# Kernel optimization log

Measured on AMD Instinct MI355X. Metric: run time of the kernel, lower is better.

## Reference

```python
import jax, jax.numpy as jnp
import numpy as np

INPUT_SIZE = 64
HIDDEN_SIZE = 512
OUTPUT_SIZE = 1
BATCH = 128
SEQ = 1024


def setup_inputs() -> dict:
    key = jax.random.key(0)
    ks = jax.random.split(key, 7)
    H, I, O = HIDDEN_SIZE, INPUT_SIZE, OUTPUT_SIZE
    s = 1.0 / np.sqrt(H)  # PyTorch LSTM init scale
    x = jax.random.normal(ks[0], (BATCH, SEQ, I), dtype=jnp.float32)
    W_ih = jax.random.uniform(ks[1], (4 * H, I), minval=-s, maxval=s, dtype=jnp.float32)
    W_hh = jax.random.uniform(ks[2], (4 * H, H), minval=-s, maxval=s, dtype=jnp.float32)
    b_ih = jax.random.uniform(ks[3], (4 * H,), minval=-s, maxval=s, dtype=jnp.float32)
    b_hh = jax.random.uniform(ks[4], (4 * H,), minval=-s, maxval=s, dtype=jnp.float32)
    W_fc = jax.random.uniform(ks[5], (O, H), minval=-s, maxval=s, dtype=jnp.float32)
    b_fc = jax.random.uniform(ks[6], (O,), minval=-s, maxval=s, dtype=jnp.float32)
    return {"x": x, "W_ih": W_ih, "W_hh": W_hh, "b_ih": b_ih, "b_hh": b_hh,
            "W_fc": W_fc, "b_fc": b_fc}


def _lstm(x, W_ih, W_hh, b_ih, b_hh):
    # x: [B, T, I]; gate order in PyTorch is (i, f, g, o) along the 4H axis.
    B = x.shape[0]
    H = W_hh.shape[1]
    # Precompute input contribution for all timesteps: [B, T, 4H] -> [T, B, 4H]
    xW = jnp.einsum('bti,gi->btg', x, W_ih) + b_ih + b_hh
    xW = jnp.swapaxes(xW, 0, 1)

    def step(carry, xt):
        h, c = carry
        gates = xt + h @ W_hh.T  # [B, 4H]
        i, f, g, o = jnp.split(gates, 4, axis=-1)
        i = jax.nn.sigmoid(i)
        f = jax.nn.sigmoid(f)
        g = jnp.tanh(g)
        o = jax.nn.sigmoid(o)
        c = f * c + i * g
        h = o * jnp.tanh(c)
        return (h, c), h

    h0 = jnp.zeros((B, H), dtype=x.dtype)
    c0 = jnp.zeros((B, H), dtype=x.dtype)
    _, h_seq = jax.lax.scan(step, (h0, c0), xW)  # [T, B, H]
    return jnp.swapaxes(h_seq, 0, 1)  # [B, T, H]


def reference(x, W_ih, W_hh, b_ih, b_hh, W_fc, b_fc):
    h = _lstm(x, W_ih, W_hh, b_ih, b_hh)          # [B, T, H]
    return jnp.einsum('bth,oh->bto', h, W_fc) + b_fc  # [B, T, O]
```

## Files before the change

### kernel.cpp

```cpp
#include <hip/hip_runtime.h>

#define BB 128
#define TT 1024
#define II 64
#define HH 512
#define KK 576
#define NBLK 256
#define NTHR 256

__global__ __launch_bounds__(NTHR, 1)
void lstm_persist(const float* __restrict__ x,
                  const float* __restrict__ W_ih,
                  const float* __restrict__ W_hh,
                  const float* __restrict__ b_ih,
                  const float* __restrict__ b_hh,
                  const float* __restrict__ W_fc,
                  const float* __restrict__ b_fc,
                  float* __restrict__ out,
                  float* __restrict__ hbuf,
                  unsigned* __restrict__ bar)
{
    __shared__ float Wl[8][KK];
    __shared__ float vx[BB][68];
    __shared__ float gl[8][BB];
    __shared__ float yl[2][BB];
    __shared__ float wfc[HH];
    __shared__ float bias[8];

    const int u  = threadIdx.x;
    const int g  = blockIdx.x;
    const int j0 = g << 1;

    unsigned epoch = 0;
    unsigned* __restrict__ subc   = bar + ((g & 7) << 5);
    unsigned* __restrict__ master = bar + 256;

    for (int r = 0; r < 8; ++r) {
        const int R = (r >> 1) * HH + j0 + (r & 1);
        for (int k = u; k < KK; k += NTHR)
            Wl[r][k] = (k < II) ? W_ih[(size_t)R * II + k]
                                : W_hh[(size_t)R * HH + (k - II)];
    }
    if (u < 8) {
        const int R = (u >> 1) * HH + j0 + (u & 1);
        bias[u] = b_ih[R] + b_hh[R];
    }
    for (int k = u; k < HH; k += NTHR) wfc[k] = W_fc[k];
    if (u < BB) {
        hbuf[(size_t)u * HH + j0]     = 0.f;
        hbuf[(size_t)u * HH + j0 + 1] = 0.f;
    }

    const float bfc = b_fc[0];
    const bool  doy = (g == 0);
    const int   bA  = u & 63, bB2 = bA + 64;
    const int   rp  = u >> 6;
    const int   rA  = rp << 1, rB = rA + 1;
    const int   ub  = u & 127, ujj = u >> 7;
    float creg = 0.f;
    float4 rx[8];

#define BAR_ARRIVE() do { __threadfence(); __syncthreads();                        \
    if (u == 0) {                                                                  \
        unsigned old = __hip_atomic_fetch_add(subc, 1u, __ATOMIC_ACQ_REL,          \
                                              __HIP_MEMORY_SCOPE_AGENT);           \
        if ((old & 31u) == 31u)                                                    \
            __hip_atomic_fetch_add(master, 1u, __ATOMIC_RELEASE,                   \
                                   __HIP_MEMORY_SCOPE_AGENT);                      \
    } ++epoch; } while (0)

#define BAR_WAIT() do {                                                            \
    if (u == 0) {                                                                  \
        while (__hip_atomic_load(master, __ATOMIC_RELAXED,                         \
                                 __HIP_MEMORY_SCOPE_AGENT) < (epoch << 3))         \
            __builtin_amdgcn_s_sleep(1);                                           \
    } __syncthreads(); __threadfence(); } while (0)

    BAR_ARRIVE();
    #pragma unroll
    for (int r8 = 0; r8 < 8; ++r8) {
        const int flat = u + NTHR * r8, b = flat >> 4, q = flat & 15;
        rx[r8] = *(const float4*)(x + ((size_t)b * TT + 0) * II + (q << 2));
    }
    BAR_WAIT();

    for (int t = 0; t < TT; ++t) {
        const float* __restrict__ hsrc = hbuf + (size_t)(t & 1) * BB * HH;
        float*       __restrict__ hdst = hbuf + (size_t)((t + 1) & 1) * BB * HH;

        float a00 = 0.f, a01 = 0.f, a10 = 0.f, a11 = 0.f;
        float yacc = 0.f;

        for (int ch = 0; ch < 9; ++ch) {
            __syncthreads();
            #pragma unroll
            for (int r8 = 0; r8 < 8; ++r8) {
                const int flat = u + NTHR * r8, b = flat >> 4, q = flat & 15;
                *(float4*)&vx[b][q << 2] = rx[r8];
            }
            if (ch < 8) {
                const int k0 = ch << 6;
                #pragma unroll
                for (int r8 = 0; r8 < 8; ++r8) {
                    const int flat = u + NTHR * r8, b = flat >> 4, q = flat & 15;
                    rx[r8] = *(const float4*)(hsrc + (size_t)b * HH + k0 + (q << 2));
                }
            }
            __syncthreads();

            {
                const float* __restrict__ wra = &Wl[rA][ch << 6];
                const float* __restrict__ wrb = &Wl[rB][ch << 6];
                const float* __restrict__ va  = &vx[bA][0];
                const float* __restrict__ vb  = &vx[bB2][0];
                #pragma unroll
                for (int k4 = 0; k4 < 16; ++k4) {
                    const float4 wa = *(const float4*)(wra + (k4 << 2));
                    const float4 wb = *(const float4*)(wrb + (k4 << 2));
                    const float4 pa = *(const float4*)(va + (k4 << 2));
                    const float4 pb = *(const float4*)(vb + (k4 << 2));
                    a00 += wa.x*pa.x + wa.y*pa.y + wa.z*pa.z + wa.w*pa.w;
                    a01 += wa.x*pb.x + wa.y*pb.y + wa.z*pb.z + wa.w*pb.w;
                    a10 += wb.x*pa.x + wb.y*pa.y + wb.z*pa.z + wb.w*pa.w;
                    a11 += wb.x*pb.x + wb.y*pb.y + wb.z*pb.z + wb.w*pb.w;
                }
            }
            if (doy && t > 0 && ch > 0) {
                const float* __restrict__ wf = &wfc[((ch - 1) << 6) + (ujj << 5)];
                const float* __restrict__ vv = &vx[ub][ujj << 5];
                #pragma unroll
                for (int k4 = 0; k4 < 8; ++k4) {
                    const float4 f4 = *(const float4*)(wf + (k4 << 2));
                    const float4 v4 = *(const float4*)(vv + (k4 << 2));
                    yacc += f4.x*v4.x + f4.y*v4.y + f4.z*v4.z + f4.w*v4.w;
                }
            }
        }

        if (doy && t > 0) yl[ujj][ub] = yacc;
        gl[rA][bA]  = a00 + bias[rA];
        gl[rA][bB2] = a01 + bias[rA];
        gl[rB][bA]  = a10 + bias[rB];
        gl[rB][bB2] = a11 + bias[rB];
        __syncthreads();

        {
            const float gi = gl[0 + ujj][ub];
            const float gf = gl[2 + ujj][ub];
            const float gg = gl[4 + ujj][ub];
            const float go = gl[6 + ujj][ub];
            const float si = 1.f / (1.f + expf(-gi));
            const float sf = 1.f / (1.f + expf(-gf));
            const float tg = tanhf(gg);
            const float so = 1.f / (1.f + expf(-go));
            const float c  = sf * creg + si * tg;
            creg = c;
            hdst[(size_t)ub * HH + j0 + ujj] = so * tanhf(c);
            if (doy && t > 0 && u < BB)
                out[(size_t)u * TT + (t - 1)] = yl[0][u] + yl[1][u] + bfc;
        }

        BAR_ARRIVE();
        if (t + 1 < TT) {
            #pragma unroll
            for (int r8 = 0; r8 < 8; ++r8) {
                const int flat = u + NTHR * r8, b = flat >> 4, q = flat & 15;
                rx[r8] = *(const float4*)(x + ((size_t)b * TT + (t + 1)) * II + (q << 2));
            }
        }
        BAR_WAIT();
    }

    if (doy) {
        const float* __restrict__ hsrc = hbuf + (size_t)(TT & 1) * BB * HH;
        float yacc = 0.f;
        for (int ch = 1; ch < 9; ++ch) {
            const int k0 = (ch - 1) << 6;
            __syncthreads();
            #pragma unroll
            for (int r8 = 0; r8 < 8; ++r8) {
                const int flat = u + NTHR * r8, b = flat >> 4, q = flat & 15;
                *(float4*)&vx[b][q << 2] =
                    *(const float4*)(hsrc + (size_t)b * HH + k0 + (q << 2));
            }
            __syncthreads();
            const float* __restrict__ wf = &wfc[((ch - 1) << 6) + (ujj << 5)];
            const float* __restrict__ vv = &vx[ub][ujj << 5];
            #pragma unroll
            for (int k4 = 0; k4 < 8; ++k4) {
                const float4 f4 = *(const float4*)(wf + (k4 << 2));
                const float4 v4 = *(const float4*)(vv + (k4 << 2));
                yacc += f4.x*v4.x + f4.y*v4.y + f4.z*v4.z + f4.w*v4.w;
            }
        }
        yl[ujj][ub] = yacc;
        __syncthreads();
        if (u < BB) out[(size_t)u * TT + (TT - 1)] = yl[0][u] + yl[1][u] + bfc;
    }
#undef BAR_ARRIVE
#undef BAR_WAIT
}

extern "C" void kernel_launch(void* const* d_in, const int* in_sizes, int n_in,
                              void* d_out, int out_size, void* d_ws, size_t ws_size,
                              hipStream_t stream) {
    (void)in_sizes; (void)n_in; (void)out_size; (void)ws_size;
    const float* x    = (const float*)d_in[0];
    const float* W_ih = (const float*)d_in[1];
    const float* W_hh = (const float*)d_in[2];
    const float* b_ih = (const float*)d_in[3];
    const float* b_hh = (const float*)d_in[4];
    const float* W_fc = (const float*)d_in[5];
    const float* b_fc = (const float*)d_in[6];
    float* out = (float*)d_out;

    unsigned* bar  = (unsigned*)d_ws;
    float*    hbuf = (float*)((char*)d_ws + 4096);

    hipMemsetAsync(d_ws, 0, 4096, stream);

    void* args[] = {(void*)&x, (void*)&W_ih, (void*)&W_hh, (void*)&b_ih,
                    (void*)&b_hh, (void*)&W_fc, (void*)&b_fc, (void*)&out,
                    (void*)&hbuf, (void*)&bar};
    hipError_t e = hipLaunchCooperativeKernel((const void*)lstm_persist,
                                              dim3(NBLK), dim3(NTHR), args, 0, stream);
    if (e != hipSuccess) {
        hipLaunchKernelGGL(lstm_persist, dim3(NBLK), dim3(NTHR), 0, stream,
                           x, W_ih, W_hh, b_ih, b_hh, W_fc, b_fc, out, hbuf, bar);
    }
}
```

Baseline: 82.62 ms.

## Replace hierarchical atomic grid barrier with per-block flags and transpose h buffer

Swaps the two-level atomic counter barrier for per-block epoch flags: each block publishes its step count, and every thread polls one block's flag, which drops the serialized arrive/master chain. The hidden state buffer becomes [H][B] with relaxed agent-scope atomic loads and stores, so each thread reads 32 coalesced values per chunk into ping-pong registers. The h zero-init moves to a host memset. Relaxed atomics with no explicit fences may leave memory ordering between blocks under-specified, and the extra per-element atomic loads could cost bandwidth.

Result: slower. 315.3 ms (+281.7%).

```diff
diff --git a/kernel.cpp b/kernel.cpp
--- a/kernel.cpp
+++ b/kernel.cpp
@@ -7,6 +7,8 @@
 #define KK 576
 #define NBLK 256
 #define NTHR 256
+
+typedef unsigned int u32;
 
 __global__ __launch_bounds__(NTHR, 1)
 void lstm_persist(const float* __restrict__ x,
@@ -18,7 +20,7 @@
                   const float* __restrict__ b_fc,
                   float* __restrict__ out,
                   float* __restrict__ hbuf,
-                  unsigned* __restrict__ bar)
+                  u32*   __restrict__ flags)
 {
     __shared__ float Wl[8][KK];
     __shared__ float vx[BB][68];
@@ -31,10 +33,6 @@
     const int g  = blockIdx.x;
     const int j0 = g << 1;
 
-    unsigned epoch = 0;
-    unsigned* __restrict__ subc   = bar + ((g & 7) << 5);
-    unsigned* __restrict__ master = bar + 256;
-
     for (int r = 0; r < 8; ++r) {
         const int R = (r >> 1) * HH + j0 + (r & 1);
         for (int k = u; k < KK; k += NTHR)
@@ -46,10 +44,6 @@
         bias[u] = b_ih[R] + b_hh[R];
     }
     for (int k = u; k < HH; k += NTHR) wfc[k] = W_fc[k];
-    if (u < BB) {
-        hbuf[(size_t)u * HH + j0]     = 0.f;
-        hbuf[(size_t)u * HH + j0 + 1] = 0.f;
-    }
 
     const float bfc = b_fc[0];
     const bool  doy = (g == 0);
@@ -57,85 +51,75 @@
     const int   rp  = u >> 6;
     const int   rA  = rp << 1, rB = rA + 1;
     const int   ub  = u & 127, ujj = u >> 7;
+    const int   xb  = u >> 4, xq = u & 15;
+    const int   b2  = u & 127;
+    const int   kk0 = (u >> 7) << 5;
     float creg = 0.f;
-    float4 rx[8];
-
-#define BAR_ARRIVE() do { __threadfence(); __syncthreads();                        \
-    if (u == 0) {                                                                  \
-        unsigned old = __hip_atomic_fetch_add(subc, 1u, __ATOMIC_ACQ_REL,          \
-                                              __HIP_MEMORY_SCOPE_AGENT);           \
-        if ((old & 31u) == 31u)                                                    \
-            __hip_atomic_fetch_add(master, 1u, __ATOMIC_RELEASE,                   \
-                                   __HIP_MEMORY_SCOPE_AGENT);                      \
-    } ++epoch; } while (0)
-
-#define BAR_WAIT() do {                                                            \
-    if (u == 0) {                                                                  \
-        while (__hip_atomic_load(master, __ATOMIC_RELAXED,                         \
-                                 __HIP_MEMORY_SCOPE_AGENT) < (epoch << 3))         \
-            __builtin_amdgcn_s_sleep(1);                                           \
-    } __syncthreads(); __threadfence(); } while (0)
-
-    BAR_ARRIVE();
-    #pragma unroll
-    for (int r8 = 0; r8 < 8; ++r8) {
-        const int flat = u + NTHR * r8, b = flat >> 4, q = flat & 15;
-        rx[r8] = *(const float4*)(x + ((size_t)b * TT + 0) * II + (q << 2));
-    }
-    BAR_WAIT();
+    float4 rx4[8];
+    float  rhA[32], rhB[32];
+
+#define LOAD_X(T) { _Pragma("unroll")                                             \
+    for (int r8 = 0; r8 < 8; ++r8)                                                \
+        rx4[r8] = *(const float4*)(x + ((size_t)(xb + 16*r8) * TT + (T)) * II     \
+                                     + (xq << 2)); }
+
+#define STAGE_X { _Pragma("unroll")                                               \
+    for (int r8 = 0; r8 < 8; ++r8)                                                \
+        *(float4*)&vx[xb + 16*r8][xq << 2] = rx4[r8]; }
+
+#define LOAD_H(R, N) { const float* hp_ = hsrc + ((size_t)(((N)-1) << 6) + kk0) * BB + b2; \
+    _Pragma("unroll")                                                             \
+    for (int i = 0; i < 32; ++i)                                                  \
+        (R)[i] = __hip_atomic_load(hp_ + (size_t)i * BB, __ATOMIC_RELAXED,        \
+                                   __HIP_MEMORY_SCOPE_AGENT); }
+
+#define STAGE_H(R) { _Pragma("unroll")                                            \
+    for (int j = 0; j < 8; ++j) {                                                 \
+        float4 f_; f_.x=(R)[4*j]; f_.y=(R)[4*j+1]; f_.z=(R)[4*j+2]; f_.w=(R)[4*j+3]; \
+        *(float4*)&vx[b2][kk0 + (j << 2)] = f_; } }
+
+#define COMPUTE(CH) {                                                             \
+    const float* wra_ = &Wl[rA][(CH) << 6];                                       \
+    const float* wrb_ = &Wl[rB][(CH) << 6];                                       \
+    const float* va_  = &vx[bA][0];                                               \
+    const float* vb_  = &vx[bB2][0];                                              \
+    _Pragma("unroll")                                                             \
+    for (int k4 = 0; k4 < 16; ++k4) {                                             \
+        const float4 wa = *(const float4*)(wra_ + (k4 << 2));                     \
+        const float4 wb = *(const float4*)(wrb_ + (k4 << 2));                     \
+        const float4 pa = *(const float4*)(va_ + (k4 << 2));                      \
+        const float4 pb = *(const float4*)(vb_ + (k4 << 2));                      \
+        a00 += wa.x*pa.x + wa.y*pa.y + wa.z*pa.z + wa.w*pa.w;                     \
+        a01 += wa.x*pb.x + wa.y*pb.y + wa.z*pb.z + wa.w*pb.w;                     \
+        a10 += wb.x*pa.x + wb.y*pa.y + wb.z*pa.z + wb.w*pa.w;                     \
+        a11 += wb.x*pb.x + wb.y*pb.y + wb.z*pb.z + wb.w*pb.w; } }
+
+#define YPART(CH) if (doy && t > 0) {                                             \
+    const float* wf_ = &wfc[(((CH)-1) << 6) + (ujj << 5)];                        \
+    const float* vv_ = &vx[ub][ujj << 5];                                         \
+    _Pragma("unroll")                                                             \
+    for (int k4 = 0; k4 < 8; ++k4) {                                              \
+        const float4 f4 = *(const float4*)(wf_ + (k4 << 2));                      \
+        const float4 v4 = *(const float4*)(vv_ + (k4 << 2));                      \
+        yacc += f4.x*v4.x + f4.y*v4.y + f4.z*v4.z + f4.w*v4.w; } }
+
+    LOAD_X(0);
 
     for (int t = 0; t < TT; ++t) {
-        const float* __restrict__ hsrc = hbuf + (size_t)(t & 1) * BB * HH;
-        float*       __restrict__ hdst = hbuf + (size_t)((t + 1) & 1) * BB * HH;
-
-        float a00 = 0.f, a01 = 0.f, a10 = 0.f, a11 = 0.f;
-        float yacc = 0.f;
-
-        for (int ch = 0; ch < 9; ++ch) {
-            __syncthreads();
-            #pragma unroll
-            for (int r8 = 0; r8 < 8; ++r8) {
-                const int flat = u + NTHR * r8, b = flat >> 4, q = flat & 15;
-                *(float4*)&vx[b][q << 2] = rx[r8];
-            }
-            if (ch < 8) {
-                const int k0 = ch << 6;
-                #pragma unroll
-                for (int r8 = 0; r8 < 8; ++r8) {
-                    const int flat = u + NTHR * r8, b = flat >> 4, q = flat & 15;
-                    rx[r8] = *(const float4*)(hsrc + (size_t)b * HH + k0 + (q << 2));
-                }
-            }
-            __syncthreads();
-
-            {
-                const float* __restrict__ wra = &Wl[rA][ch << 6];
-                const float* __restrict__ wrb = &Wl[rB][ch << 6];
-                const float* __restrict__ va  = &vx[bA][0];
-                const float* __restrict__ vb  = &vx[bB2][0];
-                #pragma unroll
-                for (int k4 = 0; k4 < 16; ++k4) {
-                    const float4 wa = *(const float4*)(wra + (k4 << 2));
-                    const float4 wb = *(const float4*)(wrb + (k4 << 2));
-                    const float4 pa = *(const float4*)(va + (k4 << 2));
-                    const float4 pb = *(const float4*)(vb + (k4 << 2));
-                    a00 += wa.x*pa.x + wa.y*pa.y + wa.z*pa.z + wa.w*pa.w;
-                    a01 += wa.x*pb.x + wa.y*pb.y + wa.z*pb.z + wa.w*pb.w;
-                    a10 += wb.x*pa.x + wb.y*pa.y + wb.z*pa.z + wb.w*pa.w;
-                    a11 += wb.x*pb.x + wb.y*pb.y + wb.z*pb.z + wb.w*pb.w;
-                }
-            }
-            if (doy && t > 0 && ch > 0) {
-                const float* __restrict__ wf = &wfc[((ch - 1) << 6) + (ujj << 5)];
-                const float* __restrict__ vv = &vx[ub][ujj << 5];
-                #pragma unroll
-                for (int k4 = 0; k4 < 8; ++k4) {
-                    const float4 f4 = *(const float4*)(wf + (k4 << 2));
-                    const float4 v4 = *(const float4*)(vv + (k4 << 2));
-                    yacc += f4.x*v4.x + f4.y*v4.y + f4.z*v4.z + f4.w*v4.w;
-                }
-            }
-        }
+        const float* __restrict__ hsrc = hbuf + (size_t)(t & 1) * HH * BB;
+        float*       __restrict__ hdst = hbuf + (size_t)((t + 1) & 1) * HH * BB;
+
+        float a00 = 0.f, a01 = 0.f, a10 = 0.f, a11 = 0.f, yacc = 0.f;
+
+        __syncthreads(); STAGE_X;        __syncthreads(); LOAD_H(rhA, 1); COMPUTE(0);
+        __syncthreads(); STAGE_H(rhA);   __syncthreads(); LOAD_H(rhB, 2); COMPUTE(1); YPART(1);
+        __syncthreads(); STAGE_H(rhB);   __syncthreads(); LOAD_H(rhA, 3); COMPUTE(2); YPART(2);
+        __syncthreads(); STAGE_H(rhA);   __syncthreads(); LOAD_H(rhB, 4); COMPUTE(3); YPART(3);
+        __syncthreads(); STAGE_H(rhB);   __syncthreads(); LOAD_H(rhA, 5); COMPUTE(4); YPART(4);
+        __syncthreads(); STAGE_H(rhA);   __syncthreads(); LOAD_H(rhB, 6); COMPUTE(5); YPART(5);
+        __syncthreads(); STAGE_H(rhB);   __syncthreads(); LOAD_H(rhA, 7); COMPUTE(6); YPART(6);
+        __syncthreads(); STAGE_H(rhA);   __syncthreads(); LOAD_H(rhB, 8); COMPUTE(7); YPART(7);
+        __syncthreads(); STAGE_H(rhB);   __syncthreads();                 COMPUTE(8); YPART(8);
 
         if (doy && t > 0) yl[ujj][ub] = yacc;
         gl[rA][bA]  = a00 + bias[rA];
@@ -155,41 +139,42 @@
             const float so = 1.f / (1.f + expf(-go));
             const float c  = sf * creg + si * tg;
             creg = c;
-            hdst[(size_t)ub * HH + j0 + ujj] = so * tanhf(c);
+            const float hval = so * tanhf(c);
+            __hip_atomic_store(hdst + (size_t)(j0 + ujj) * BB + ub, hval,
+                               __ATOMIC_RELAXED, __HIP_MEMORY_SCOPE_AGENT);
             if (doy && t > 0 && u < BB)
                 out[(size_t)u * TT + (t - 1)] = yl[0][u] + yl[1][u] + bfc;
         }
 
-        BAR_ARRIVE();
-        if (t + 1 < TT) {
-            #pragma unroll
-            for (int r8 = 0; r8 < 8; ++r8) {
-                const int flat = u + NTHR * r8, b = flat >> 4, q = flat & 15;
-                rx[r8] = *(const float4*)(x + ((size_t)b * TT + (t + 1)) * II + (q << 2));
-            }
+        __syncthreads();
+        if (u == 0)
+            __hip_atomic_store(&flags[g], (u32)(t + 1),
+                               __ATOMIC_RELAXED, __HIP_MEMORY_SCOPE_AGENT);
+        if (t + 1 < TT) LOAD_X(t + 1);
+        if (t + 1 < TT || doy) {
+            const u32 want = (u32)(t + 1);
+            while (__hip_atomic_load(&flags[u], __ATOMIC_RELAXED,
+                                     __HIP_MEMORY_SCOPE_AGENT) < want)
+                __builtin_amdgcn_s_sleep(1);
         }
-        BAR_WAIT();
+        __syncthreads();
     }
 
     if (doy) {
-        const float* __restrict__ hsrc = hbuf + (size_t)(TT & 1) * BB * HH;
+        const float* __restrict__ hsrc = hbuf + (size_t)(TT & 1) * HH * BB;
         float yacc = 0.f;
-        for (int ch = 1; ch < 9; ++ch) {
-            const int k0 = (ch - 1) << 6;
+        #pragma unroll 1
+        for (int n = 1; n <= 8; ++n) {
             __syncthreads();
-            #pragma unroll
-            for (int r8 = 0; r8 < 8; ++r8) {
-                const int flat = u + NTHR * r8, b = flat >> 4, q = flat & 15;
-                *(float4*)&vx[b][q << 2] =
-                    *(const float4*)(hsrc + (size_t)b * HH + k0 + (q << 2));
-            }
+            LOAD_H(rhA, n);
+            STAGE_H(rhA);
             __syncthreads();
-            const float* __restrict__ wf = &wfc[((ch - 1) << 6) + (ujj << 5)];
-            const float* __restrict__ vv = &vx[ub][ujj << 5];
+            const float* wf_ = &wfc[((n - 1) << 6) + (ujj << 5)];
+            const float* vv_ = &vx[ub][ujj << 5];
             #pragma unroll
             for (int k4 = 0; k4 < 8; ++k4) {
-                const float4 f4 = *(const float4*)(wf + (k4 << 2));
-                const float4 v4 = *(const float4*)(vv + (k4 << 2));
+                const float4 f4 = *(const float4*)(wf_ + (k4 << 2));
+                const float4 v4 = *(const float4*)(vv_ + (k4 << 2));
                 yacc += f4.x*v4.x + f4.y*v4.y + f4.z*v4.z + f4.w*v4.w;
             }
         }
@@ -197,8 +182,12 @@
         __syncthreads();
         if (u < BB) out[(size_t)u * TT + (TT - 1)] = yl[0][u] + yl[1][u] + bfc;
     }
-#undef BAR_ARRIVE
-#undef BAR_WAIT
+#undef LOAD_X
+#undef STAGE_X
+#undef LOAD_H
+#undef STAGE_H
+#undef COMPUTE
+#undef YPART
 }
 
 extern "C" void kernel_launch(void* const* d_in, const int* in_sizes, int n_in,
@@ -214,18 +203,18 @@
     const float* b_fc = (const float*)d_in[6];
     float* out = (float*)d_out;
 
-    unsigned* bar  = (unsigned*)d_ws;
-    float*    hbuf = (float*)((char*)d_ws + 4096);
-
-    hipMemsetAsync(d_ws, 0, 4096, stream);
+    u32*   flags = (u32*)d_ws;
+    float* hbuf  = (float*)((char*)d_ws + 4096);
+
+    hipMemsetAsync(d_ws, 0, 4096 + (size_t)HH * BB * sizeof(float), stream);
 
     void* args[] = {(void*)&x, (void*)&W_ih, (void*)&W_hh, (void*)&b_ih,
                     (void*)&b_hh, (void*)&W_fc, (void*)&b_fc, (void*)&out,
-                    (void*)&hbuf, (void*)&bar};
+                    (void*)&hbuf, (void*)&flags};
     hipError_t e = hipLaunchCooperativeKernel((const void*)lstm_persist,
                                               dim3(NBLK), dim3(NTHR), args, 0, stream);
     if (e != hipSuccess) {
         hipLaunchKernelGGL(lstm_persist, dim3(NBLK), dim3(NTHR), 0, stream,
-                           x, W_ih, W_hh, b_ih, b_hh, W_fc, b_fc, out, hbuf, bar);
+                           x, W_ih, W_hh, b_ih, b_hh, W_fc, b_fc, out, hbuf, flags);
     }
 }
```
